# Kernel optimization log

Hardware: AMD Instinct MI355X
Metric: run time of the kernel (lower is better)

The kernel has to match this reference:

```python
import jax, jax.numpy as jnp
from jax import lax
import numpy as np
import math


def make_kernel():
    # StyleGAN2 blur kernel [1,3,3,1], normalized outer product
    k = jnp.array([1.0, 3.0, 3.0, 1.0], dtype=jnp.float32)
    k2 = jnp.outer(k, k)
    return k2 / jnp.sum(k2)


def upfirdn2d(x, kernel, up=1, pad=(0, 0)):
    # x: [B,C,H,W]; depthwise FIR filter, optional zero-insert upsampling
    C = x.shape[1]
    w = jnp.tile(jnp.flip(kernel)[None, None].astype(x.dtype), (C, 1, 1, 1))
    # torch upfirdn pads up-1 trailing zeros after the last sample; lhs_dilation
    # only inserts zeros between samples, so fold the extra zeros into pad[1].
    p = (pad[0], pad[1] + up - 1)
    return lax.conv_general_dilated(
        x, w, (1, 1), (p, p), lhs_dilation=(up, up), feature_group_count=C)


def modulated_conv(x, weight, style, demodulate=True, up=False):
    # per-sample weight modulation + demodulation, executed as grouped conv
    B, Cin, H, W = x.shape
    Cout, _, k, _ = weight.shape
    scale = 1.0 / math.sqrt(Cin * k * k)
    w = scale * weight[None] * style[:, None, :, None, None]  # [B,Cout,Cin,k,k]
    if demodulate:
        d = lax.rsqrt(jnp.sum(w * w, axis=(2, 3, 4)) + 1e-8)
        w = w * d[:, :, None, None, None]
    xg = x.reshape(1, B * Cin, H, W)
    if up:
        # conv_transpose2d(stride=2, pad=0) == lhs-dilated conv with flipped kernel
        wg = jnp.flip(w, (-2, -1)).reshape(B * Cout, Cin, k, k)
        out = lax.conv_general_dilated(
            xg, wg, (1, 1), ((k - 1, k - 1), (k - 1, k - 1)),
            lhs_dilation=(2, 2), feature_group_count=B)
    else:
        pad = k // 2
        out = lax.conv_general_dilated(
            xg, w.reshape(B * Cout, Cin, k, k), (1, 1),
            ((pad, pad), (pad, pad)), feature_group_count=B)
    return out.reshape(B, Cout, out.shape[2], out.shape[3])


def fused_lrelu(x, bias):
    y = x + bias[None, :, None, None]
    return jnp.where(y >= 0, y, 0.2 * y) * math.sqrt(2.0)


def setup_inputs() -> dict:
    key = jax.random.key(0)
    ks = jax.random.split(key, 12)
    B, C, H = 8, 512, 32
    f = jnp.float32
    return {
        "x": jax.random.normal(ks[0], (B, C, H, H), f),
        "skip": jax.random.normal(ks[1], (B, 3, H, H), f),
        "w1": jax.random.normal(ks[2], (C, C, 3, 3), f),
        "b1": jnp.zeros((C,), f),
        "s1": jax.random.normal(ks[3], (B, C), f),
        "nw1": jax.random.normal(ks[4], (1,), f) * 0.1,
        "n1": jax.random.normal(ks[5], (B, 1, 2 * H, 2 * H), f),
        "w2": jax.random.normal(ks[6], (C, C, 3, 3), f),
        "b2": jnp.zeros((C,), f),
        "s2": jax.random.normal(ks[7], (B, C), f),
        "nw2": jax.random.normal(ks[8], (1,), f) * 0.1,
        "n2": jax.random.normal(ks[9], (B, 1, 2 * H, 2 * H), f),
        "w_rgb": jax.random.normal(ks[10], (3, C, 1, 1), f),
        "b_rgb": jnp.zeros((3,), f),
        "s_rgb": jax.random.normal(ks[11], (B, C), f),
    }


def reference(x, skip, w1, b1, s1, nw1, n1, w2, b2, s2, nw2, n2,
              w_rgb, b_rgb, s_rgb):
    kern = make_kernel()
    # conv1: upsampling modulated conv + blur (Blur with upsample_factor=2)
    out = modulated_conv(x, w1, s1, demodulate=True, up=True)
    out = upfirdn2d(out, kern * 4.0, up=1, pad=(1, 1))
    out = out + nw1 * n1          # NoiseInjection
    out = fused_lrelu(out, b1)    # FusedLeakyReLU
    # conv2: plain modulated conv
    out = modulated_conv(out, w2, s2, demodulate=True)
    out = out + nw2 * n2
    out = fused_lrelu(out, b2)
    # ToRGB: 1x1 mod conv, no demodulation, + bias; skip = rgb + upsample(skip)
    rgb = modulated_conv(out, w_rgb, s_rgb, demodulate=False)
    rgb = rgb + b_rgb[None, :, None, None]
    skip_up = upfirdn2d(skip, kern * 4.0, up=2, pad=(2, 1))
    return rgb + skip_up
```

## Files before the change

kernel.cpp:

```cpp
#include <hip/hip_runtime.h>
#include <stdint.h>

typedef unsigned short ushort_t;
typedef unsigned int uint_t;
typedef __bf16 bf16x8 __attribute__((ext_vector_type(8)));
typedef float f32x4 __attribute__((ext_vector_type(4)));

#define GLOBAL_AS __attribute__((address_space(1)))
#define LDS_AS    __attribute__((address_space(3)))

#define SCALE_CONV 0.014731391f
#define SCALE_RGB  0.044194174f
#define SQRT2_F    1.41421356237f

__device__ __forceinline__ void async_cp16(const void* g, void* l) {
  __builtin_amdgcn_global_load_lds((const GLOBAL_AS uint_t*)g,
                                   (LDS_AS uint_t*)l, 16, 0, 0);
}
__device__ __forceinline__ ushort_t f2bf(float v) {
  union { float f; uint_t u; } c; c.f = v;
  uint_t r = c.u + 0x7fffu + ((c.u >> 16) & 1u);
  return (ushort_t)(r >> 16);
}
__device__ __forceinline__ float bf2f(ushort_t u) {
  union { uint_t u; float f; } c; c.u = ((uint_t)u) << 16;
  return c.f;
}

__global__ __launch_bounds__(256) void prep_x1(
    const float* __restrict__ x, const float* __restrict__ s1,
    ushort_t* __restrict__ xpad) {
  __shared__ ushort_t t[32 * 520];
  const int b  = blockIdx.x >> 5;
  const int j1 = blockIdx.x & 31;
  for (int idx = threadIdx.x; idx < 512 * 32; idx += 256) {
    int ci = idx >> 5, j2 = idx & 31;
    float v = x[(size_t)(b * 512 + ci) * 1024 + j1 * 32 + j2];
    v *= s1[b * 512 + ci] * SCALE_CONV;
    t[j2 * 520 + ci] = f2bf(v);
  }
  __syncthreads();
  for (int idx = threadIdx.x; idx < 32 * 512; idx += 256) {
    int j2 = idx >> 9, ci = idx & 511;
    xpad[((size_t)(b * 34 + j1 + 1) * 34 + (j2 + 1)) * 512 + ci] = t[j2 * 520 + ci];
  }
}

__global__ __launch_bounds__(256) void prep_w(
    const float* __restrict__ w1, const float* __restrict__ w2,
    ushort_t* __restrict__ wt1, ushort_t* __restrict__ wt2,
    float* __restrict__ wsqT1, float* __restrict__ wsqT2) {
  int t = blockIdx.x * 256 + threadIdx.x;
  const float* w  = (t < 262144) ? w1 : w2;
  ushort_t*   wt  = (t < 262144) ? wt1 : wt2;
  float*      wq  = (t < 262144) ? wsqT1 : wsqT2;
  int tt = t & 262143;
  int ci = tt & 511, co = tt >> 9;
  const float* wp = w + (size_t)(co * 512 + ci) * 9;
  float sq = 0.f;
#pragma unroll
  for (int u = 0; u < 9; ++u) {
    float v = wp[u];
    sq += v * v;
    wt[((size_t)u * 512 + co) * 512 + ci] = f2bf(v);
  }
  wq[ci * 512 + co] = sq;
}

__global__ __launch_bounds__(512) void demod2(
    const float* __restrict__ wsqT1, const float* __restrict__ s1, float* __restrict__ d1,
    const float* __restrict__ wsqT2, const float* __restrict__ s2, float* __restrict__ d2) {
  const float* wq = blockIdx.y ? wsqT2 : wsqT1;
  const float* s  = blockIdx.y ? s2 : s1;
  float*       d  = blockIdx.y ? d2 : d1;
  const int b  = blockIdx.x;
  const int co = threadIdx.x;
  __shared__ float ssq[512];
  float sv = s[b * 512 + co];
  ssq[co] = sv * sv;
  __syncthreads();
  float a = 0.f;
#pragma unroll 4
  for (int ci = 0; ci < 512; ++ci) a += wq[ci * 512 + co] * ssq[ci];
  d[b * 512 + co] = rsqrtf(a * (1.f / 4608.f) + 1e-8f);
}

__global__ __launch_bounds__(256) void border_zero(
    ushort_t* __restrict__ xpad, ushort_t* __restrict__ ypad, ushort_t* __restrict__ opad) {
  const int z = blockIdx.z;
  ushort_t* p = (z == 0) ? xpad : (z == 1 ? ypad : opad);
  const int W = (z == 0) ? 34 : (z == 1 ? 67 : 66);
  const int nb = 4 * W - 4;
  const int t = blockIdx.x * 256 + threadIdx.x;
  const int pix = t >> 6, ch = (t & 63) * 8;
  if (pix >= nb) return;
  const int b = blockIdx.y;
  int y, x;
  if (pix < W)          { y = 0;     x = pix; }
  else if (pix < 2 * W) { y = W - 1; x = pix - W; }
  else { int q = pix - 2 * W; y = 1 + (q >> 1); x = (q & 1) ? W - 1 : 0; }
  uint4 z4 = {0, 0, 0, 0};
  *(uint4*)(p + ((size_t)(b * W + y) * W + x) * 512 + ch) = z4;
}

__constant__ int           c_ph_off[4]  = {0, 4, 6, 8};
__constant__ int           c_ph_ntap[4] = {4, 2, 2, 1};
__constant__ unsigned char c_tap_u1[9]  = {0,0,1,1, 0,1, 1,1, 1};
__constant__ unsigned char c_tap_u2[9]  = {0,1,0,1, 1,1, 0,1, 1};
__constant__ unsigned char c_tap_pl[9]  = {8,6,2,0, 7,1, 5,3, 4};

__global__ __launch_bounds__(256, 4) void gemm_conv1(
    const ushort_t* __restrict__ inp, const ushort_t* __restrict__ wt,
    const float* __restrict__ dmod, ushort_t* __restrict__ outp) {
  __shared__ ushort_t ldsA[128 * 64];
  __shared__ ushort_t ldsB[128 * 64];

  const int tid  = threadIdx.x;
  const int lane = tid & 63;
  const int wv   = tid >> 6;
  const int wm   = wv & 1;
  const int wn   = wv >> 1;
  const int l16  = lane & 15;
  const int quad = lane >> 4;

  const int mtile = blockIdx.x;
  const int ntile = blockIdx.y;
  const int a  = blockIdx.z;
  const int a1 = a >> 1, a2 = a & 1;

  const int cl = ((lane & 7) - (lane >> 3)) & 7;
  const char* pA[4];
  const char* pB[4];
#pragma unroll
  for (int t = 0; t < 4; ++t) {
    int row = wv * 32 + t * 8 + (lane >> 3);
    int m   = mtile * 128 + row;
    if (m > 8711) m = 8711;
    int b = m / 1089, rr = m % 1089;
    int p1 = rr / 33, p2 = rr % 33;
    size_t pix = ((size_t)(b * 34 + p1) * 34 + p2) * 512;
    pA[t] = (const char*)inp + pix * 2 + cl * 16;
    int n = ntile * 128 + row;
    pB[t] = (const char*)wt + (size_t)n * 1024 + cl * 16;
  }
  char* dstA[4];
  char* dstB[4];
#pragma unroll
  for (int t = 0; t < 4; ++t) {
    dstA[t] = (char*)ldsA + wv * 4096 + t * 1024;
    dstB[t] = (char*)ldsB + wv * 4096 + t * 1024;
  }

  int offA[4], offB[4];
#pragma unroll
  for (int i = 0; i < 4; ++i) {
    int r  = wm * 64 + i * 16 + l16;
    int rn = wn * 64 + i * 16 + l16;
    offA[i] = r  * 64 + (((quad + r)  & 7) << 3);
    offB[i] = rn * 64 + (((quad + rn) & 7) << 3);
  }

  f32x4 acc[4][4];
#pragma unroll
  for (int i = 0; i < 4; ++i)
#pragma unroll
    for (int j = 0; j < 4; ++j) acc[i][j] = (f32x4){0.f, 0.f, 0.f, 0.f};

  const int ntap = c_ph_ntap[a];
#pragma unroll 1
  for (int ti = 0; ti < ntap; ++ti) {
    int e = c_ph_off[a] + ti;
    int aoff = ((int)c_tap_u1[e] * 34 + (int)c_tap_u2[e]) * 1024;
    int boff = (int)c_tap_pl[e] * 524288;
#pragma unroll 1
    for (int kc = 0; kc < 8; ++kc) {
      const int koff = kc * 128;
      __syncthreads();
#pragma unroll
      for (int t = 0; t < 4; ++t) async_cp16(pA[t] + aoff + koff, dstA[t]);
#pragma unroll
      for (int t = 0; t < 4; ++t) async_cp16(pB[t] + boff + koff, dstB[t]);
      __syncthreads();
#pragma unroll
      for (int kk = 0; kk < 2; ++kk) {
        const int kx = kk << 5;
        bf16x8 af[4], bg[4];
#pragma unroll
        for (int i = 0; i < 4; ++i) af[i] = *reinterpret_cast<const bf16x8*>(ldsA + (offA[i] ^ kx));
#pragma unroll
        for (int j = 0; j < 4; ++j) bg[j] = *reinterpret_cast<const bf16x8*>(ldsB + (offB[j] ^ kx));
#pragma unroll
        for (int i = 0; i < 4; ++i)
#pragma unroll
          for (int j = 0; j < 4; ++j)
            acc[i][j] = __builtin_amdgcn_mfma_f32_16x16x32_bf16(af[i], bg[j], acc[i][j], 0, 0, 0);
      }
    }
  }

  int co_[4];
#pragma unroll
  for (int j = 0; j < 4; ++j) co_[j] = ntile * 128 + wn * 64 + j * 16 + l16;

#pragma unroll
  for (int i = 0; i < 4; ++i) {
#pragma unroll
    for (int r = 0; r < 4; ++r) {
      int m = mtile * 128 + wm * 64 + i * 16 + quad * 4 + r;
      if (m < 8712) {
        int b = m / 1089, rr = m % 1089;
        int p1 = rr / 33, p2 = rr % 33;
        if ((a1 == 0 || p1 < 32) && (a2 == 0 || p2 < 32)) {
          int o1 = 2 * p1 + a1, o2 = 2 * p2 + a2;
          size_t ob = ((size_t)(b * 67 + o1 + 1) * 67 + (o2 + 1)) * 512;
#pragma unroll
          for (int j = 0; j < 4; ++j)
            outp[ob + co_[j]] = f2bf(acc[i][j][r] * dmod[b * 512 + co_[j]]);
        }
      }
    }
  }
}

__global__ __launch_bounds__(256, 4) void gemm_conv2(
    const ushort_t* __restrict__ inp, const ushort_t* __restrict__ wt,
    const float* __restrict__ dmod, const float* __restrict__ noise,
    const float* __restrict__ nw, const float* __restrict__ bias,
    const float* __restrict__ srgb, const float* __restrict__ wrgb,
    float* __restrict__ rgbpart) {
  __shared__ ushort_t ldsA[128 * 64];
  __shared__ ushort_t ldsB[128 * 64];

  const int tid  = threadIdx.x;
  const int lane = tid & 63;
  const int wv   = tid >> 6;
  const int wm   = wv & 1;
  const int wn   = wv >> 1;
  const int l16  = lane & 15;
  const int quad = lane >> 4;

  const int mtile = blockIdx.x;
  const int ntile = blockIdx.y;

  const int cl = ((lane & 7) - (lane >> 3)) & 7;
  const char* pA[4];
  const char* pB[4];
#pragma unroll
  for (int t = 0; t < 4; ++t) {
    int row = wv * 32 + t * 8 + (lane >> 3);
    int m   = mtile * 128 + row;
    int b = m >> 12, o1 = (m >> 6) & 63, o2 = m & 63;
    size_t pix = ((size_t)(b * 66 + o1 + 1) * 66 + (o2 + 1)) * 512;
    pA[t] = (const char*)inp + pix * 2 + cl * 16;
    int n = ntile * 128 + row;
    pB[t] = (const char*)wt + (size_t)n * 1024 + cl * 16;
  }
  char* dstA[4];
  char* dstB[4];
#pragma unroll
  for (int t = 0; t < 4; ++t) {
    dstA[t] = (char*)ldsA + wv * 4096 + t * 1024;
    dstB[t] = (char*)ldsB + wv * 4096 + t * 1024;
  }

  int offA[4], offB[4];
#pragma unroll
  for (int i = 0; i < 4; ++i) {
    int r  = wm * 64 + i * 16 + l16;
    int rn = wn * 64 + i * 16 + l16;
    offA[i] = r  * 64 + (((quad + r)  & 7) << 3);
    offB[i] = rn * 64 + (((quad + rn) & 7) << 3);
  }

  f32x4 acc[4][4];
#pragma unroll
  for (int i = 0; i < 4; ++i)
#pragma unroll
    for (int j = 0; j < 4; ++j) acc[i][j] = (f32x4){0.f, 0.f, 0.f, 0.f};

#pragma unroll 1
  for (int ti = 0; ti < 9; ++ti) {
    int aoff = ((ti / 3 - 1) * 66 + (ti % 3 - 1)) * 1024;
    int boff = ti * 524288;
#pragma unroll 1
    for (int kc = 0; kc < 8; ++kc) {
      const int koff = kc * 128;
      __syncthreads();
#pragma unroll
      for (int t = 0; t < 4; ++t) async_cp16(pA[t] + aoff + koff, dstA[t]);
#pragma unroll
      for (int t = 0; t < 4; ++t) async_cp16(pB[t] + boff + koff, dstB[t]);
      __syncthreads();
#pragma unroll
      for (int kk = 0; kk < 2; ++kk) {
        const int kx = kk << 5;
        bf16x8 af[4], bg[4];
#pragma unroll
        for (int i = 0; i < 4; ++i) af[i] = *reinterpret_cast<const bf16x8*>(ldsA + (offA[i] ^ kx));
#pragma unroll
        for (int j = 0; j < 4; ++j) bg[j] = *reinterpret_cast<const bf16x8*>(ldsB + (offB[j] ^ kx));
#pragma unroll
        for (int i = 0; i < 4; ++i)
#pragma unroll
          for (int j = 0; j < 4; ++j)
            acc[i][j] = __builtin_amdgcn_mfma_f32_16x16x32_bf16(af[i], bg[j], acc[i][j], 0, 0, 0);
      }
    }
  }

  const int b = mtile >> 5;
  int co_[4];
#pragma unroll
  for (int j = 0; j < 4; ++j) co_[j] = ntile * 128 + wn * 64 + j * 16 + l16;
  const float nwv = nw[0];
  float dj_[4], sj_[4], bj_[4], wr[3][4];
#pragma unroll
  for (int j = 0; j < 4; ++j) {
    dj_[j] = dmod[b * 512 + co_[j]];
    sj_[j] = srgb[b * 512 + co_[j]] * SCALE_RGB;
    bj_[j] = bias[co_[j]];
#pragma unroll
    for (int c = 0; c < 3; ++c) wr[c][j] = wrgb[c * 512 + co_[j]];
  }
#pragma unroll
  for (int i = 0; i < 4; ++i) {
#pragma unroll
    for (int r = 0; r < 4; ++r) {
      int m = mtile * 128 + wm * 64 + i * 16 + quad * 4 + r;
      int o1 = (m >> 6) & 63, o2 = m & 63;
      float nz = nwv * noise[(b << 12) + (o1 << 6) + o2];
      float vv[4];
#pragma unroll
      for (int j = 0; j < 4; ++j) {
        float v = acc[i][j][r] * dj_[j] + nz + bj_[j];
        v = (v >= 0.f ? v : 0.2f * v) * SQRT2_F;
        vv[j] = v * sj_[j];
      }
#pragma unroll
      for (int c = 0; c < 3; ++c) {
        float s = vv[0] * wr[c][0] + vv[1] * wr[c][1] + vv[2] * wr[c][2] + vv[3] * wr[c][3];
        s += __shfl_xor(s, 1);
        s += __shfl_xor(s, 2);
        s += __shfl_xor(s, 4);
        s += __shfl_xor(s, 8);
        if (l16 == 0) atomicAdd(&rgbpart[c * 32768 + m], s);
      }
    }
  }
}

__global__ __launch_bounds__(256) void blur_noise_act(
    const ushort_t* __restrict__ y1pad, const float* __restrict__ noise,
    const float* __restrict__ nw, const float* __restrict__ bias,
    const float* __restrict__ s2, ushort_t* __restrict__ out1pad) {
  const int cg  = threadIdx.x & 63;
  const int pg  = blockIdx.x * 4 + (threadIdx.x >> 6);
  const int b   = pg >> 10;
  const int q1  = (pg >> 4) & 63;
  const int q2g = (pg & 15) * 4;
  const float cw[4] = {0.25f, 0.75f, 0.75f, 0.25f};

  float acc[4][8];
#pragma unroll
  for (int j = 0; j < 4; ++j)
#pragma unroll
    for (int e = 0; e < 8; ++e) acc[j][e] = 0.f;

#pragma unroll
  for (int t2 = 0; t2 < 7; ++t2) {
    int cc = q2g + t2;
    float vt[8];
#pragma unroll
    for (int e = 0; e < 8; ++e) vt[e] = 0.f;
#pragma unroll
    for (int t1 = 0; t1 < 4; ++t1) {
      const ushort_t* p = y1pad + ((size_t)(b * 67 + q1 + t1) * 67 + cc) * 512 + cg * 8;
      ushort_t v[8];
      *(uint4*)v = *(const uint4*)p;
#pragma unroll
      for (int e = 0; e < 8; ++e) vt[e] += cw[t1] * bf2f(v[e]);
    }
#pragma unroll
    for (int j = 0; j < 4; ++j) {
      int t = t2 - j;
      if (t >= 0 && t < 4) {
#pragma unroll
        for (int e = 0; e < 8; ++e) acc[j][e] += cw[t] * vt[e];
      }
    }
  }

  const float nwv = nw[0];
  float bj[8], sj[8];
#pragma unroll
  for (int e = 0; e < 8; ++e) {
    bj[e] = bias[cg * 8 + e];
    sj[e] = s2[b * 512 + cg * 8 + e] * SCALE_CONV;
  }
#pragma unroll
  for (int j = 0; j < 4; ++j) {
    int q2 = q2g + j;
    float nz = nwv * noise[(b << 12) + (q1 << 6) + q2];
    ushort_t o[8];
#pragma unroll
    for (int e = 0; e < 8; ++e) {
      float v = acc[j][e] + nz + bj[e];
      v = (v >= 0.f ? v : 0.2f * v) * SQRT2_F * sj[e];
      o[e] = f2bf(v);
    }
    *(uint4*)(out1pad + ((size_t)(b * 66 + q1 + 1) * 66 + (q2 + 1)) * 512 + cg * 8) = *(uint4*)o;
  }
}

__global__ __launch_bounds__(256) void rgb_finish(
    const float* __restrict__ rgbpart, const float* __restrict__ brgb,
    const float* __restrict__ skip, float* __restrict__ out) {
  const int t = blockIdx.x * 256 + threadIdx.x;
  if (t >= 98304) return;
  const int m = t & 32767, c = t >> 15;
  const int b = m >> 12, o1 = (m >> 6) & 63, o2 = m & 63;
  int P1 = o1 >> 1, P2 = o2 >> 1;
  int jy0, jy1, jx0, jx1;
  float wy0, wy1, wx0, wx1;
  if ((o1 & 1) == 0) { jy0 = P1 - 1; wy0 = .25f; jy1 = P1;     wy1 = .75f; }
  else               { jy0 = P1;     wy0 = .75f; jy1 = P1 + 1; wy1 = .25f; }
  if ((o2 & 1) == 0) { jx0 = P2 - 1; wx0 = .25f; jx1 = P2;     wx1 = .75f; }
  else               { jx0 = P2;     wx0 = .75f; jx1 = P2 + 1; wx1 = .25f; }
  const float* sp = skip + (size_t)(b * 3 + c) * 1024;
  float sv = 0.f;
  if (jy0 >= 0 && jy0 < 32) {
    if (jx0 >= 0 && jx0 < 32) sv += wy0 * wx0 * sp[jy0 * 32 + jx0];
    if (jx1 >= 0 && jx1 < 32) sv += wy0 * wx1 * sp[jy0 * 32 + jx1];
  }
  if (jy1 >= 0 && jy1 < 32) {
    if (jx0 >= 0 && jx0 < 32) sv += wy1 * wx0 * sp[jy1 * 32 + jx0];
    if (jx1 >= 0 && jx1 < 32) sv += wy1 * wx1 * sp[jy1 * 32 + jx1];
  }
  out[((size_t)(b * 3 + c) << 12) + (o1 << 6) + o2] = rgbpart[c * 32768 + m] + brgb[c] + sv;
}

extern "C" void kernel_launch(void* const* d_in, const int* in_sizes, int n_in,
                              void* d_out, int out_size, void* d_ws, size_t ws_size,
                              hipStream_t stream) {
  const float* x    = (const float*)d_in[0];
  const float* skip = (const float*)d_in[1];
  const float* w1   = (const float*)d_in[2];
  const float* b1   = (const float*)d_in[3];
  const float* s1   = (const float*)d_in[4];
  const float* nw1  = (const float*)d_in[5];
  const float* n1   = (const float*)d_in[6];
  const float* w2   = (const float*)d_in[7];
  const float* b2   = (const float*)d_in[8];
  const float* s2   = (const float*)d_in[9];
  const float* nw2  = (const float*)d_in[10];
  const float* n2   = (const float*)d_in[11];
  const float* wrgb = (const float*)d_in[12];
  const float* brgb = (const float*)d_in[13];
  const float* srgb = (const float*)d_in[14];

  char* ws = (char*)d_ws;
  const size_t XPAD_B  = (size_t)8 * 34 * 34 * 512 * 2;
  const size_t Y1PAD_B = (size_t)8 * 67 * 67 * 512 * 2;
  const size_t OUT1_B  = (size_t)8 * 66 * 66 * 512 * 2;
  const size_t WT_B    = (size_t)9 * 512 * 512 * 2;
  size_t off = 0;
  ushort_t* xpad1   = (ushort_t*)(ws + off); off += XPAD_B;
  ushort_t* y1pad   = (ushort_t*)(ws + off); off += Y1PAD_B;
  ushort_t* out1pad = (ushort_t*)(ws + off); off += OUT1_B;
  ushort_t* wt1     = (ushort_t*)(ws + off); off += WT_B;
  ushort_t* wt2     = (ushort_t*)(ws + off); off += WT_B;
  float*    d1      = (float*)(ws + off);    off += 8 * 512 * 4;
  float*    d2      = (float*)(ws + off);    off += 8 * 512 * 4;
  float*    rgbpart = (float*)(ws + off);    off += 3 * 32768 * 4;
  float*    wsqT1  = (float*)y1pad;
  float*    wsqT2  = wsqT1 + 512 * 512;

  hipMemsetAsync(rgbpart, 0, 3 * 32768 * 4, stream);
  prep_x1<<<256, 256, 0, stream>>>(x, s1, xpad1);
  prep_w<<<2048, 256, 0, stream>>>(w1, w2, wt1, wt2, wsqT1, wsqT2);
  demod2<<<dim3(8, 2), 512, 0, stream>>>(wsqT1, s1, d1, wsqT2, s2, d2);
  border_zero<<<dim3(66, 8, 3), 256, 0, stream>>>(xpad1, y1pad, out1pad);

  gemm_conv1<<<dim3(69, 4, 4), 256, 0, stream>>>(xpad1, wt1, d1, y1pad);
  blur_noise_act<<<2048, 256, 0, stream>>>(y1pad, n1, nw1, b1, s2, out1pad);
  gemm_conv2<<<dim3(256, 4), 256, 0, stream>>>(
      out1pad, wt2, d2, n2, nw2, b2, srgb, wrgb, rgbpart);
  rgb_finish<<<384, 256, 0, stream>>>(rgbpart, brgb, skip, (float*)d_out);
}
```

Baseline: 392.1 us.

## Merge prep kernels, widen demod, swizzle GEMM tiles, enlarge blur strips

Merges prep_x1 and prep_w into one launch and folds the rgbpart memset into border_zero, so fewer launches are issued. The demod kernel now splits the input-channel reduction across 128 blocks instead of 16 for more parallelism. Both GEMMs use a 1D grid with grouped tile ordering (8 m-tiles share n-tiles) for better L2 reuse, and their launch-bounds occupancy hint drops from 4 to 3. Blur now computes 8 outputs per thread, which reuses column loads but uses more registers.

```diff
diff --git a/kernel.cpp b/kernel.cpp
--- a/kernel.cpp
+++ b/kernel.cpp
@@ -27,30 +27,30 @@
   return c.f;
 }
 
-__global__ __launch_bounds__(256) void prep_x1(
+__global__ __launch_bounds__(256) void prep_all(
     const float* __restrict__ x, const float* __restrict__ s1,
-    ushort_t* __restrict__ xpad) {
-  __shared__ ushort_t t[32 * 520];
-  const int b  = blockIdx.x >> 5;
-  const int j1 = blockIdx.x & 31;
-  for (int idx = threadIdx.x; idx < 512 * 32; idx += 256) {
-    int ci = idx >> 5, j2 = idx & 31;
-    float v = x[(size_t)(b * 512 + ci) * 1024 + j1 * 32 + j2];
-    v *= s1[b * 512 + ci] * SCALE_CONV;
-    t[j2 * 520 + ci] = f2bf(v);
-  }
-  __syncthreads();
-  for (int idx = threadIdx.x; idx < 32 * 512; idx += 256) {
-    int j2 = idx >> 9, ci = idx & 511;
-    xpad[((size_t)(b * 34 + j1 + 1) * 34 + (j2 + 1)) * 512 + ci] = t[j2 * 520 + ci];
-  }
-}
-
-__global__ __launch_bounds__(256) void prep_w(
+    ushort_t* __restrict__ xpad,
     const float* __restrict__ w1, const float* __restrict__ w2,
     ushort_t* __restrict__ wt1, ushort_t* __restrict__ wt2,
     float* __restrict__ wsqT1, float* __restrict__ wsqT2) {
-  int t = blockIdx.x * 256 + threadIdx.x;
+  if (blockIdx.x < 256) {
+    __shared__ ushort_t t[32 * 520];
+    const int b  = blockIdx.x >> 5;
+    const int j1 = blockIdx.x & 31;
+    for (int idx = threadIdx.x; idx < 512 * 32; idx += 256) {
+      int ci = idx >> 5, j2 = idx & 31;
+      float v = x[(size_t)(b * 512 + ci) * 1024 + j1 * 32 + j2];
+      v *= s1[b * 512 + ci] * SCALE_CONV;
+      t[j2 * 520 + ci] = f2bf(v);
+    }
+    __syncthreads();
+    for (int idx = threadIdx.x; idx < 32 * 512; idx += 256) {
+      int j2 = idx >> 9, ci = idx & 511;
+      xpad[((size_t)(b * 34 + j1 + 1) * 34 + (j2 + 1)) * 512 + ci] = t[j2 * 520 + ci];
+    }
+    return;
+  }
+  int t = (blockIdx.x - 256) * 256 + threadIdx.x;
   const float* w  = (t < 262144) ? w1 : w2;
   ushort_t*   wt  = (t < 262144) ? wt1 : wt2;
   float*      wq  = (t < 262144) ? wsqT1 : wsqT2;
@@ -67,27 +67,47 @@
   wq[ci * 512 + co] = sq;
 }
 
-__global__ __launch_bounds__(512) void demod2(
+__global__ __launch_bounds__(256) void demod3(
     const float* __restrict__ wsqT1, const float* __restrict__ s1, float* __restrict__ d1,
     const float* __restrict__ wsqT2, const float* __restrict__ s2, float* __restrict__ d2) {
-  const float* wq = blockIdx.y ? wsqT2 : wsqT1;
-  const float* s  = blockIdx.y ? s2 : s1;
-  float*       d  = blockIdx.y ? d2 : d1;
-  const int b  = blockIdx.x;
-  const int co = threadIdx.x;
+  const float* wq = blockIdx.z ? wsqT2 : wsqT1;
+  const float* s  = blockIdx.z ? s2 : s1;
+  float*       d  = blockIdx.z ? d2 : d1;
+  const int b   = blockIdx.y;
+  const int co  = blockIdx.x * 64 + (threadIdx.x & 63);
+  const int cig = threadIdx.x >> 6;
   __shared__ float ssq[512];
-  float sv = s[b * 512 + co];
-  ssq[co] = sv * sv;
+  __shared__ float red[4][64];
+  for (int i = threadIdx.x; i < 512; i += 256) {
+    float v = s[b * 512 + i];
+    ssq[i] = v * v;
+  }
   __syncthreads();
   float a = 0.f;
 #pragma unroll 4
-  for (int ci = 0; ci < 512; ++ci) a += wq[ci * 512 + co] * ssq[ci];
-  d[b * 512 + co] = rsqrtf(a * (1.f / 4608.f) + 1e-8f);
+  for (int ci = cig * 128; ci < cig * 128 + 128; ++ci)
+    a += wq[ci * 512 + co] * ssq[ci];
+  red[cig][threadIdx.x & 63] = a;
+  __syncthreads();
+  if (cig == 0) {
+    int l = threadIdx.x & 63;
+    float tot = red[0][l] + red[1][l] + red[2][l] + red[3][l];
+    d[b * 512 + co] = rsqrtf(tot * (1.f / 4608.f) + 1e-8f);
+  }
 }
 
 __global__ __launch_bounds__(256) void border_zero(
-    ushort_t* __restrict__ xpad, ushort_t* __restrict__ ypad, ushort_t* __restrict__ opad) {
+    ushort_t* __restrict__ xpad, ushort_t* __restrict__ ypad, ushort_t* __restrict__ opad,
+    float* __restrict__ rgbpart) {
   const int z = blockIdx.z;
+  if (z == 3) {
+    int i = (blockIdx.y * 66 + blockIdx.x) * 256 + threadIdx.x;
+    if (i < 24576) {
+      uint4 z4 = {0, 0, 0, 0};
+      *(uint4*)(rgbpart + i * 4) = z4;
+    }
+    return;
+  }
   ushort_t* p = (z == 0) ? xpad : (z == 1 ? ypad : opad);
   const int W = (z == 0) ? 34 : (z == 1 ? 67 : 66);
   const int nb = 4 * W - 4;
@@ -109,9 +129,17 @@
 __constant__ unsigned char c_tap_u2[9]  = {0,1,0,1, 1,1, 0,1, 1};
 __constant__ unsigned char c_tap_pl[9]  = {8,6,2,0, 7,1, 5,3, 4};
 
-__global__ __launch_bounds__(256, 4) void gemm_conv1(
+__global__ __launch_bounds__(256, 3) void gemm_conv1(
     const ushort_t* __restrict__ inp, const ushort_t* __restrict__ wt,
     const float* __restrict__ dmod, ushort_t* __restrict__ outp) {
+  const int g = blockIdx.x;
+  const int mtile = ((g >> 7) << 3) | (g & 7);
+  if (mtile >= 69) return;
+  const int sub   = (g >> 3) & 15;
+  const int a     = sub >> 2;
+  const int ntile = sub & 3;
+  const int a1 = a >> 1, a2 = a & 1;
+
   __shared__ ushort_t ldsA[128 * 64];
   __shared__ ushort_t ldsB[128 * 64];
 
@@ -122,11 +150,6 @@
   const int wn   = wv >> 1;
   const int l16  = lane & 15;
   const int quad = lane >> 4;
-
-  const int mtile = blockIdx.x;
-  const int ntile = blockIdx.y;
-  const int a  = blockIdx.z;
-  const int a1 = a >> 1, a2 = a & 1;
 
   const int cl = ((lane & 7) - (lane >> 3)) & 7;
   const char* pA[4];
@@ -222,12 +245,16 @@
   }
 }
 
-__global__ __launch_bounds__(256, 4) void gemm_conv2(
+__global__ __launch_bounds__(256, 3) void gemm_conv2(
     const ushort_t* __restrict__ inp, const ushort_t* __restrict__ wt,
     const float* __restrict__ dmod, const float* __restrict__ noise,
     const float* __restrict__ nw, const float* __restrict__ bias,
     const float* __restrict__ srgb, const float* __restrict__ wrgb,
     float* __restrict__ rgbpart) {
+  const int g = blockIdx.x;
+  const int mtile = ((g >> 5) << 3) | (g & 7);
+  const int ntile = (g >> 3) & 3;
+
   __shared__ ushort_t ldsA[128 * 64];
   __shared__ ushort_t ldsB[128 * 64];
 
@@ -238,9 +265,6 @@
   const int wn   = wv >> 1;
   const int l16  = lane & 15;
   const int quad = lane >> 4;
-
-  const int mtile = blockIdx.x;
-  const int ntile = blockIdx.y;
 
   const int cl = ((lane & 7) - (lane >> 3)) & 7;
   const char* pA[4];
@@ -355,19 +379,19 @@
     const float* __restrict__ s2, ushort_t* __restrict__ out1pad) {
   const int cg  = threadIdx.x & 63;
   const int pg  = blockIdx.x * 4 + (threadIdx.x >> 6);
-  const int b   = pg >> 10;
-  const int q1  = (pg >> 4) & 63;
-  const int q2g = (pg & 15) * 4;
+  const int b   = pg >> 9;
+  const int q1  = (pg >> 3) & 63;
+  const int q2g = (pg & 7) * 8;
   const float cw[4] = {0.25f, 0.75f, 0.75f, 0.25f};
 
-  float acc[4][8];
-#pragma unroll
-  for (int j = 0; j < 4; ++j)
+  float acc[8][8];
+#pragma unroll
+  for (int j = 0; j < 8; ++j)
 #pragma unroll
     for (int e = 0; e < 8; ++e) acc[j][e] = 0.f;
 
 #pragma unroll
-  for (int t2 = 0; t2 < 7; ++t2) {
+  for (int t2 = 0; t2 < 11; ++t2) {
     int cc = q2g + t2;
     float vt[8];
 #pragma unroll
@@ -381,7 +405,7 @@
       for (int e = 0; e < 8; ++e) vt[e] += cw[t1] * bf2f(v[e]);
     }
 #pragma unroll
-    for (int j = 0; j < 4; ++j) {
+    for (int j = 0; j < 8; ++j) {
       int t = t2 - j;
       if (t >= 0 && t < 4) {
 #pragma unroll
@@ -398,7 +422,7 @@
     sj[e] = s2[b * 512 + cg * 8 + e] * SCALE_CONV;
   }
 #pragma unroll
-  for (int j = 0; j < 4; ++j) {
+  for (int j = 0; j < 8; ++j) {
     int q2 = q2g + j;
     float nz = nwv * noise[(b << 12) + (q1 << 6) + q2];
     ushort_t o[8];
@@ -475,15 +499,13 @@
   float*    wsqT1  = (float*)y1pad;
   float*    wsqT2  = wsqT1 + 512 * 512;
 
-  hipMemsetAsync(rgbpart, 0, 3 * 32768 * 4, stream);
-  prep_x1<<<256, 256, 0, stream>>>(x, s1, xpad1);
-  prep_w<<<2048, 256, 0, stream>>>(w1, w2, wt1, wt2, wsqT1, wsqT2);
-  demod2<<<dim3(8, 2), 512, 0, stream>>>(wsqT1, s1, d1, wsqT2, s2, d2);
-  border_zero<<<dim3(66, 8, 3), 256, 0, stream>>>(xpad1, y1pad, out1pad);
-
-  gemm_conv1<<<dim3(69, 4, 4), 256, 0, stream>>>(xpad1, wt1, d1, y1pad);
-  blur_noise_act<<<2048, 256, 0, stream>>>(y1pad, n1, nw1, b1, s2, out1pad);
-  gemm_conv2<<<dim3(256, 4), 256, 0, stream>>>(
+  prep_all<<<2304, 256, 0, stream>>>(x, s1, xpad1, w1, w2, wt1, wt2, wsqT1, wsqT2);
+  demod3<<<dim3(8, 8, 2), 256, 0, stream>>>(wsqT1, s1, d1, wsqT2, s2, d2);
+  border_zero<<<dim3(66, 8, 4), 256, 0, stream>>>(xpad1, y1pad, out1pad, rgbpart);
+
+  gemm_conv1<<<1152, 256, 0, stream>>>(xpad1, wt1, d1, y1pad);
+  blur_noise_act<<<1024, 256, 0, stream>>>(y1pad, n1, nw1, b1, s2, out1pad);
+  gemm_conv2<<<1024, 256, 0, stream>>>(
       out1pad, wt2, d2, n2, nw2, b2, srgb, wrgb, rgbpart);
   rgb_finish<<<384, 256, 0, stream>>>(rgbpart, brgb, skip, (float*)d_out);
 }
```

New measurement: 375.8 us. 4.2% less time.
